# Performance work log

Hardware: AMD Instinct MI355X
Metric: run time of the kernel (lower is better)

## Reference

```python
import jax, jax.numpy as jnp
import numpy as np

N = 50000       # nodes
E = 800000      # edges
F_IN = 128      # num_node_features
H = 128         # hidden_channels
C = 10          # num_classes
G = 512         # graphs in batch


def _glorot(key, shape):
    fan_in, fan_out = shape
    lim = float(np.sqrt(6.0 / (fan_in + fan_out)))
    return jax.random.uniform(key, shape, jnp.float32, -lim, lim)


def setup_inputs() -> dict:
    key = jax.random.key(0)
    ks = jax.random.split(key, 12)
    x = jax.random.normal(ks[0], (N, F_IN), jnp.float32)
    edge_index = jax.random.randint(ks[1], (2, E), 0, N, dtype=jnp.int32).astype(jnp.int64)
    batch = jnp.sort(jax.random.randint(ks[2], (N,), 0, G, dtype=jnp.int32)).astype(jnp.int64)
    return {
        "x": x,
        "edge_index": edge_index,
        "batch": batch,
        "W1": _glorot(ks[3], (F_IN, H)), "b1": jnp.zeros((H,), jnp.float32),
        "W2": _glorot(ks[4], (H, H)),    "b2": jnp.zeros((H,), jnp.float32),
        "W3": _glorot(ks[5], (H, H)),    "b3": jnp.zeros((H,), jnp.float32),
        "W_lin": _glorot(ks[6], (H, C)), "b_lin": jnp.zeros((C,), jnp.float32),
    }


def _gcn_conv(h_in, W, b, src, dst, dis):
    # GCNConv: D^{-1/2} (A + I) D^{-1/2} (X W) + b  (symmetric norm, self-loops)
    h = h_in @ W                                   # [N, H]
    coef = (dis[src] * dis[dst])[:, None]          # [E, 1]
    msg = h[src] * coef                            # gather + scale
    agg = jax.ops.segment_sum(msg, dst, num_segments=N)  # scatter-add at targets
    agg = agg + h * (dis * dis)[:, None]           # self-loop term
    return agg + b


def reference(x, edge_index, batch, W1, b1, W2, b2, W3, b3, W_lin, b_lin):
    src, dst = edge_index[0], edge_index[1]
    # degree with self-loops (counted at aggregation target, PyG convention)
    deg = jax.ops.segment_sum(jnp.ones((E,), jnp.float32), dst, num_segments=N) + 1.0
    dis = jax.lax.rsqrt(deg)

    h = jax.nn.relu(_gcn_conv(x, W1, b1, src, dst, dis))
    h = jax.nn.relu(_gcn_conv(h, W2, b2, src, dst, dis))
    h = _gcn_conv(h, W3, b3, src, dst, dis)

    # global mean pool over graphs
    counts = jax.ops.segment_sum(jnp.ones((N,), jnp.float32), batch, num_segments=G)
    pooled = jax.ops.segment_sum(h, batch, num_segments=G)
    pooled = pooled / jnp.maximum(counts, 1.0)[:, None]

    # dropout(p=0.5, training=False) -> identity
    return pooled @ W_lin + b_lin
```

## Files before the change

kernel.cpp:

```cpp
#include <hip/hip_runtime.h>

#define NN 50000
#define NE 800000
#define FD 128
#define NG 512
#define NC 10

#define NBUCK 196
#define BSHIFT 8
#define BSTRIDE 5120
#define P1_EPB 4096
#define P1_BLOCKS ((NE + P1_EPB - 1) / P1_EPB)

typedef __attribute__((ext_vector_type(8))) short bf16x8;
typedef __attribute__((ext_vector_type(4))) float f32x4;


__device__ __forceinline__ unsigned short f2bf(float f) {
  unsigned int b = __float_as_uint(f);
  b += 0x7FFF + ((b >> 16) & 1);
  return (unsigned short)(b >> 16);
}
__device__ __forceinline__ float blo(unsigned int u) {
  return __uint_as_float(u << 16);
}
__device__ __forceinline__ float bhi(unsigned int u) {
  return __uint_as_float(u & 0xFFFF0000u);
}


__global__ __launch_bounds__(256) void setup_kernel(const float* __restrict__ W1,
                                                    const float* __restrict__ W2,
                                                    const float* __restrict__ W3,
                                                    unsigned short* __restrict__ wf1,
                                                    unsigned short* __restrict__ wf2,
                                                    unsigned short* __restrict__ wf3,
                                                    int* __restrict__ gcursor) {
  int idx = blockIdx.x * 256 + threadIdx.x;
  if (idx < 3 * 16384) {
    int wi = idx >> 14;
    int i = idx & 16383;
    const float* W = (wi == 0) ? W1 : (wi == 1) ? W2 : W3;
    unsigned short* wf = (wi == 0) ? wf1 : (wi == 1) ? wf2 : wf3;
    int j = i & 7, l = (i >> 3) & 63, ks = (i >> 9) & 3, ct = i >> 11;
    int k = ks * 32 + (l >> 4) * 8 + j;
    int c = ct * 16 + (l & 15);
    float w = W[k * 128 + c];
    unsigned int bb = __float_as_uint(w);
    unsigned int bh = bb & 0xFFFF0000u;
    float r = w - __uint_as_float(bh);
    int base = (((ct * 4 + ks) * 2 + 0) * 64 + l) * 8 + j;
    wf[base] = (unsigned short)(bh >> 16);
    wf[base + 512] = f2bf(r);
  } else {
    int t = idx - 3 * 16384;
    if (t < NBUCK) gcursor[t] = t * BSTRIDE;
  }
}
#define SETUP_BLOCKS ((3 * 16384 + NBUCK + 255) / 256)

__global__ __launch_bounds__(1024) void pass1_kernel(const int* __restrict__ ei,
                                                     int* __restrict__ gcursor,
                                                     unsigned int* __restrict__ bucketBuf) {
  __shared__ int bh[NBUCK];
  __shared__ int gbase[NBUCK];
  __shared__ int bcur[NBUCK];

  int tid = threadIdx.x;
  int e0 = blockIdx.x * P1_EPB;
  int ne = NE - e0; if (ne > P1_EPB) ne = P1_EPB;

  if (tid < NBUCK) bh[tid] = 0;
  __syncthreads();

  for (int i = tid; i < ne; i += 1024) {
    int d = ei[NE + e0 + i];
    atomicAdd(&bh[d >> BSHIFT], 1);
  }
  __syncthreads();

  if (tid < NBUCK) {
    bcur[tid] = 0;
    gbase[tid] = (bh[tid] > 0) ? atomicAdd(&gcursor[tid], bh[tid]) : 0;
  }
  __syncthreads();

  for (int i = tid; i < ne; i += 1024) {
    int s = ei[e0 + i];
    int d = ei[NE + e0 + i];
    int b = d >> BSHIFT;
    int p = atomicAdd(&bcur[b], 1);
    bucketBuf[gbase[b] + p] = (unsigned int)s | ((unsigned int)d << 16);
  }
}

__global__ __launch_bounds__(1024) void pass2_kernel(const unsigned int* __restrict__ bucketBuf,
                                                     const int* __restrict__ gcur,
                                                     int* __restrict__ offs,
                                                     float* __restrict__ dis,
                                                     unsigned short* __restrict__ csr) {
  __shared__ unsigned int raw[BSTRIDE];
  __shared__ unsigned short sorted[BSTRIDE];
  __shared__ int h[256], pos[256], cur[256];
  __shared__ int sarr[256];

  int b = blockIdx.x;
  int tid = threadIdx.x;
  int nStart = b << BSHIFT;

  if (tid < 256) sarr[tid] = (tid < NBUCK) ? (gcur[tid] - tid * BSTRIDE) : 0;
  __syncthreads();
  #pragma unroll
  for (int off = 1; off < 256; off <<= 1) {
    int v = 0;
    if (tid < 256 && tid >= off) v = sarr[tid - off];
    __syncthreads();
    if (tid < 256) sarr[tid] += v;
    __syncthreads();
  }
  int cntb = gcur[b] - b * BSTRIDE;
  int cnt = (cntb > BSTRIDE) ? BSTRIDE : cntb;
  int eStart = sarr[b] - cntb;
  if (b == NBUCK - 1 && tid == 0) offs[NN] = sarr[NBUCK - 1];

  for (int i = tid; i < cnt; i += 1024) raw[i] = bucketBuf[(size_t)b * BSTRIDE + i];
  if (tid < 256) h[tid] = 0;
  __syncthreads();

  for (int i = tid; i < cnt; i += 1024) atomicAdd(&h[(raw[i] >> 16) - nStart], 1);
  __syncthreads();

  if (tid < 256) pos[tid] = h[tid];
  __syncthreads();
  #pragma unroll
  for (int off = 1; off < 256; off <<= 1) {
    int v = 0;
    if (tid < 256 && tid >= off) v = pos[tid - off];
    __syncthreads();
    if (tid < 256) pos[tid] += v;
    __syncthreads();
  }
  if (tid < 256) {
    int ex = pos[tid] - h[tid];
    cur[tid] = ex;
    int n = nStart + tid;
    if (n < NN) {
      offs[n] = eStart + ex;
      dis[n] = rsqrtf((float)h[tid] + 1.0f);
    }
  }
  __syncthreads();

  for (int i = tid; i < cnt; i += 1024) {
    unsigned int r = raw[i];
    int d = (int)(r >> 16) - nStart;
    int p = atomicAdd(&cur[d], 1);
    sorted[p] = (unsigned short)(r & 0xFFFFu);
  }
  __syncthreads();

  for (int i = tid; i < cnt; i += 1024) csr[eStart + i] = sorted[i];
}


__global__ __launch_bounds__(256) void gemm_f32_kernel(const float* __restrict__ A,
                                                       const unsigned short* __restrict__ wf,
                                                       const float* __restrict__ dis,
                                                       unsigned short* __restrict__ Hs) {
  __shared__ unsigned short ldsW[32768];
  int tid = threadIdx.x;
  {
    const uint4* src = reinterpret_cast<const uint4*>(wf);
    uint4* dst = reinterpret_cast<uint4*>(ldsW);
    #pragma unroll
    for (int i = 0; i < 16; ++i) dst[tid + i * 256] = src[tid + i * 256];
  }
  __syncthreads();

  int w = tid >> 6, lane = tid & 63;
  int rowbase = blockIdx.x * 128 + w * 32;
  int kgrp = lane >> 4;
  int r0 = rowbase + (lane & 15);
  int r1 = r0 + 16;
  int a0 = (r0 < NN) ? r0 : 0;
  int a1 = (r1 < NN) ? r1 : 0;

  f32x4 acc0[8], acc1[8];
  #pragma unroll
  for (int ct = 0; ct < 8; ++ct) {
    f32x4 z = {0.f, 0.f, 0.f, 0.f};
    acc0[ct] = z; acc1[ct] = z;
  }

  #pragma unroll
  for (int ks = 0; ks < 4; ++ks) {
    bf16x8 ahi0, alo0, ahi1, alo1;
    {
      const float* ap = A + (size_t)a0 * FD + ks * 32 + kgrp * 8;
      float4 v0 = *reinterpret_cast<const float4*>(ap);
      float4 v1 = *reinterpret_cast<const float4*>(ap + 4);
      float a[8] = {v0.x, v0.y, v0.z, v0.w, v1.x, v1.y, v1.z, v1.w};
      #pragma unroll
      for (int j = 0; j < 8; ++j) {
        unsigned int bb = __float_as_uint(a[j]);
        unsigned int bh = bb & 0xFFFF0000u;
        float r = a[j] - __uint_as_float(bh);
        ahi0[j] = (short)(bh >> 16);
        alo0[j] = (short)f2bf(r);
      }
    }
    {
      const float* ap = A + (size_t)a1 * FD + ks * 32 + kgrp * 8;
      float4 v0 = *reinterpret_cast<const float4*>(ap);
      float4 v1 = *reinterpret_cast<const float4*>(ap + 4);
      float a[8] = {v0.x, v0.y, v0.z, v0.w, v1.x, v1.y, v1.z, v1.w};
      #pragma unroll
      for (int j = 0; j < 8; ++j) {
        unsigned int bb = __float_as_uint(a[j]);
        unsigned int bh = bb & 0xFFFF0000u;
        float r = a[j] - __uint_as_float(bh);
        ahi1[j] = (short)(bh >> 16);
        alo1[j] = (short)f2bf(r);
      }
    }
    #pragma unroll
    for (int ct = 0; ct < 8; ++ct) {
      int off = (((ct * 4 + ks) * 2) * 64 + lane) * 8;
      bf16x8 bhiV = *reinterpret_cast<const bf16x8*>(&ldsW[off]);
      bf16x8 bloV = *reinterpret_cast<const bf16x8*>(&ldsW[off + 512]);
      acc0[ct] = __builtin_amdgcn_mfma_f32_16x16x32_bf16(ahi0, bhiV, acc0[ct], 0, 0, 0);
      acc1[ct] = __builtin_amdgcn_mfma_f32_16x16x32_bf16(ahi1, bhiV, acc1[ct], 0, 0, 0);
      acc0[ct] = __builtin_amdgcn_mfma_f32_16x16x32_bf16(alo0, bhiV, acc0[ct], 0, 0, 0);
      acc1[ct] = __builtin_amdgcn_mfma_f32_16x16x32_bf16(alo1, bhiV, acc1[ct], 0, 0, 0);
      acc0[ct] = __builtin_amdgcn_mfma_f32_16x16x32_bf16(ahi0, bloV, acc0[ct], 0, 0, 0);
      acc1[ct] = __builtin_amdgcn_mfma_f32_16x16x32_bf16(ahi1, bloV, acc1[ct], 0, 0, 0);
    }
  }

  int ccol = lane & 15;
  #pragma unroll
  for (int g = 0; g < 2; ++g) {
    int crow0 = rowbase + g * 16 + kgrp * 4;
    #pragma unroll
    for (int i = 0; i < 4; ++i) {
      int r = crow0 + i;
      if (r < NN) {
        float dv = dis[r];
        #pragma unroll
        for (int ct = 0; ct < 8; ++ct) {
          float v = g ? acc1[ct][i] : acc0[ct][i];
          Hs[(size_t)r * FD + ct * 16 + ccol] = f2bf(dv * v);
        }
      }
    }
  }
}


__global__ __launch_bounds__(256) void gemm_bf16_kernel(const unsigned short* __restrict__ Ab,
                                                        const unsigned short* __restrict__ wf,
                                                        const float* __restrict__ dis,
                                                        unsigned short* __restrict__ Hs) {
  __shared__ unsigned short ldsW[32768];
  int tid = threadIdx.x;
  {
    const uint4* src = reinterpret_cast<const uint4*>(wf);
    uint4* dst = reinterpret_cast<uint4*>(ldsW);
    #pragma unroll
    for (int i = 0; i < 16; ++i) dst[tid + i * 256] = src[tid + i * 256];
  }
  __syncthreads();

  int w = tid >> 6, lane = tid & 63;
  int rowbase = blockIdx.x * 128 + w * 32;
  int kgrp = lane >> 4;
  int r0 = rowbase + (lane & 15);
  int r1 = r0 + 16;
  int a0 = (r0 < NN) ? r0 : 0;
  int a1 = (r1 < NN) ? r1 : 0;

  f32x4 acc0[8], acc1[8];
  #pragma unroll
  for (int ct = 0; ct < 8; ++ct) {
    f32x4 z = {0.f, 0.f, 0.f, 0.f};
    acc0[ct] = z; acc1[ct] = z;
  }

  #pragma unroll
  for (int ks = 0; ks < 4; ++ks) {
    bf16x8 av0, av1;
    {
      uint4 u = *reinterpret_cast<const uint4*>(&Ab[(size_t)a0 * FD + ks * 32 + kgrp * 8]);
      unsigned int uu[4] = {u.x, u.y, u.z, u.w};
      #pragma unroll
      for (int p = 0; p < 4; ++p) {
        unsigned short lo16 = (unsigned short)(uu[p] & 0xFFFFu);
        unsigned short hi16 = (unsigned short)(uu[p] >> 16);
        av0[2 * p + 0] = (short)(((short)lo16 < 0) ? 0 : lo16);
        av0[2 * p + 1] = (short)(((short)hi16 < 0) ? 0 : hi16);
      }
    }
    {
      uint4 u = *reinterpret_cast<const uint4*>(&Ab[(size_t)a1 * FD + ks * 32 + kgrp * 8]);
      unsigned int uu[4] = {u.x, u.y, u.z, u.w};
      #pragma unroll
      for (int p = 0; p < 4; ++p) {
        unsigned short lo16 = (unsigned short)(uu[p] & 0xFFFFu);
        unsigned short hi16 = (unsigned short)(uu[p] >> 16);
        av1[2 * p + 0] = (short)(((short)lo16 < 0) ? 0 : lo16);
        av1[2 * p + 1] = (short)(((short)hi16 < 0) ? 0 : hi16);
      }
    }
    #pragma unroll
    for (int ct = 0; ct < 8; ++ct) {
      int off = (((ct * 4 + ks) * 2) * 64 + lane) * 8;
      bf16x8 bhiV = *reinterpret_cast<const bf16x8*>(&ldsW[off]);
      bf16x8 bloV = *reinterpret_cast<const bf16x8*>(&ldsW[off + 512]);
      acc0[ct] = __builtin_amdgcn_mfma_f32_16x16x32_bf16(av0, bhiV, acc0[ct], 0, 0, 0);
      acc1[ct] = __builtin_amdgcn_mfma_f32_16x16x32_bf16(av1, bhiV, acc1[ct], 0, 0, 0);
      acc0[ct] = __builtin_amdgcn_mfma_f32_16x16x32_bf16(av0, bloV, acc0[ct], 0, 0, 0);
      acc1[ct] = __builtin_amdgcn_mfma_f32_16x16x32_bf16(av1, bloV, acc1[ct], 0, 0, 0);
    }
  }

  int ccol = lane & 15;
  #pragma unroll
  for (int g = 0; g < 2; ++g) {
    int crow0 = rowbase + g * 16 + kgrp * 4;
    #pragma unroll
    for (int i = 0; i < 4; ++i) {
      int r = crow0 + i;
      if (r < NN) {
        float dv = dis[r];
        #pragma unroll
        for (int ct = 0; ct < 8; ++ct) {
          float v = g ? acc1[ct][i] : acc0[ct][i];
          Hs[(size_t)r * FD + ct * 16 + ccol] = f2bf(dv * v);
        }
      }
    }
  }
}


#define EDGE8(acc, h)                                        \
  acc[0] += blo(h.x); acc[1] += bhi(h.x);                    \
  acc[2] += blo(h.y); acc[3] += bhi(h.y);                    \
  acc[4] += blo(h.z); acc[5] += bhi(h.z);                    \
  acc[6] += blo(h.w); acc[7] += bhi(h.w);

#define EDGE8M(acc, h, m)                                    \
  acc[0] += m * blo(h.x); acc[1] += m * bhi(h.x);            \
  acc[2] += m * blo(h.y); acc[3] += m * bhi(h.y);            \
  acc[4] += m * blo(h.z); acc[5] += m * bhi(h.z);            \
  acc[6] += m * blo(h.w); acc[7] += m * bhi(h.w);

__global__ __launch_bounds__(256) void agg_edge_kernel(const int* __restrict__ offs,
                                                       const unsigned short* __restrict__ csr,
                                                       const float* __restrict__ dis,
                                                       const unsigned short* __restrict__ Hs,
                                                       const float* __restrict__ bias,
                                                       unsigned short* __restrict__ AGG) {
  int pair = blockIdx.x * 4 + (threadIdx.x >> 6);
  int n0 = pair * 2;
  if (n0 >= NN) return;
  n0 = __builtin_amdgcn_readfirstlane(n0);
  int n1 = n0 + 1;
  int lane = threadIdx.x & 63;
  int q = lane >> 4;
  int ch = (lane & 15) * 8;

  int beg0 = offs[n0], end0 = offs[n0 + 1];
  int beg1 = end0,     end1 = offs[n1 + 1];

  float a0[8], a1[8];
  #pragma unroll
  for (int k = 0; k < 8; ++k) { a0[k] = 0.f; a1[k] = 0.f; }

  if (q == 0) {
    uint4 hn = *reinterpret_cast<const uint4*>(&Hs[(size_t)n0 * FD + ch]);
    EDGE8(a0, hn);
  } else if (q == 1) {
    uint4 hn = *reinterpret_cast<const uint4*>(&Hs[(size_t)n1 * FD + ch]);
    EDGE8(a1, hn);
  }

  int j0 = beg0, j1 = beg1;
  int it = min((end0 - j0) >> 4, (end1 - j1) >> 4);
  for (int t = 0; t < it; ++t) {
    int s00 = csr[j0 + q], s01 = csr[j0 + q + 4], s02 = csr[j0 + q + 8], s03 = csr[j0 + q + 12];
    int s10 = csr[j1 + q], s11 = csr[j1 + q + 4], s12 = csr[j1 + q + 8], s13 = csr[j1 + q + 12];
    uint4 h00 = *reinterpret_cast<const uint4*>(&Hs[(size_t)s00 * FD + ch]);
    uint4 h01 = *reinterpret_cast<const uint4*>(&Hs[(size_t)s01 * FD + ch]);
    uint4 h02 = *reinterpret_cast<const uint4*>(&Hs[(size_t)s02 * FD + ch]);
    uint4 h03 = *reinterpret_cast<const uint4*>(&Hs[(size_t)s03 * FD + ch]);
    uint4 h10 = *reinterpret_cast<const uint4*>(&Hs[(size_t)s10 * FD + ch]);
    uint4 h11 = *reinterpret_cast<const uint4*>(&Hs[(size_t)s11 * FD + ch]);
    uint4 h12 = *reinterpret_cast<const uint4*>(&Hs[(size_t)s12 * FD + ch]);
    uint4 h13 = *reinterpret_cast<const uint4*>(&Hs[(size_t)s13 * FD + ch]);
    EDGE8(a0, h00); EDGE8(a0, h01); EDGE8(a0, h02); EDGE8(a0, h03);
    EDGE8(a1, h10); EDGE8(a1, h11); EDGE8(a1, h12); EDGE8(a1, h13);
    j0 += 16; j1 += 16;
  }
  for (; j0 < end0; j0 += 16) {
    int last = end0 - 1;
    int e0 = j0 + q, e1 = j0 + q + 4, e2 = j0 + q + 8, e3 = j0 + q + 12;
    int i0 = (e0 <= last) ? e0 : 0, i1 = (e1 <= last) ? e1 : 0;
    int i2 = (e2 <= last) ? e2 : 0, i3 = (e3 <= last) ? e3 : 0;
    float m0 = (e0 <= last) ? 1.f : 0.f, m1 = (e1 <= last) ? 1.f : 0.f;
    float m2 = (e2 <= last) ? 1.f : 0.f, m3 = (e3 <= last) ? 1.f : 0.f;
    int s0 = csr[i0], s1 = csr[i1], s2 = csr[i2], s3 = csr[i3];
    uint4 h0 = *reinterpret_cast<const uint4*>(&Hs[(size_t)s0 * FD + ch]);
    uint4 h1 = *reinterpret_cast<const uint4*>(&Hs[(size_t)s1 * FD + ch]);
    uint4 h2 = *reinterpret_cast<const uint4*>(&Hs[(size_t)s2 * FD + ch]);
    uint4 h3 = *reinterpret_cast<const uint4*>(&Hs[(size_t)s3 * FD + ch]);
    EDGE8M(a0, h0, m0); EDGE8M(a0, h1, m1); EDGE8M(a0, h2, m2); EDGE8M(a0, h3, m3);
  }
  for (; j1 < end1; j1 += 16) {
    int last = end1 - 1;
    int e0 = j1 + q, e1 = j1 + q + 4, e2 = j1 + q + 8, e3 = j1 + q + 12;
    int i0 = (e0 <= last) ? e0 : 0, i1 = (e1 <= last) ? e1 : 0;
    int i2 = (e2 <= last) ? e2 : 0, i3 = (e3 <= last) ? e3 : 0;
    float m0 = (e0 <= last) ? 1.f : 0.f, m1 = (e1 <= last) ? 1.f : 0.f;
    float m2 = (e2 <= last) ? 1.f : 0.f, m3 = (e3 <= last) ? 1.f : 0.f;
    int s0 = csr[i0], s1 = csr[i1], s2 = csr[i2], s3 = csr[i3];
    uint4 h0 = *reinterpret_cast<const uint4*>(&Hs[(size_t)s0 * FD + ch]);
    uint4 h1 = *reinterpret_cast<const uint4*>(&Hs[(size_t)s1 * FD + ch]);
    uint4 h2 = *reinterpret_cast<const uint4*>(&Hs[(size_t)s2 * FD + ch]);
    uint4 h3 = *reinterpret_cast<const uint4*>(&Hs[(size_t)s3 * FD + ch]);
    EDGE8M(a1, h0, m0); EDGE8M(a1, h1, m1); EDGE8M(a1, h2, m2); EDGE8M(a1, h3, m3);
  }

  #pragma unroll
  for (int k = 0; k < 8; ++k) {
    float v0 = a0[k];
    v0 += __shfl_xor(v0, 16, 64);
    v0 += __shfl_xor(v0, 32, 64);
    a0[k] = v0;
    float v1 = a1[k];
    v1 += __shfl_xor(v1, 16, 64);
    v1 += __shfl_xor(v1, 32, 64);
    a1[k] = v1;
  }

  if (q < 2) {
    int n = q ? n1 : n0;
    float dn = dis[n];
    const float* acc = q ? a1 : a0;
    float4 b0 = *reinterpret_cast<const float4*>(&bias[ch]);
    float4 b1 = *reinterpret_cast<const float4*>(&bias[ch + 4]);
    float o[8];
    o[0] = b0.x + dn * acc[0]; o[1] = b0.y + dn * acc[1];
    o[2] = b0.z + dn * acc[2]; o[3] = b0.w + dn * acc[3];
    o[4] = b1.x + dn * acc[4]; o[5] = b1.y + dn * acc[5];
    o[6] = b1.z + dn * acc[6]; o[7] = b1.w + dn * acc[7];
    uint4 pk;
    pk.x = (unsigned int)f2bf(o[0]) | ((unsigned int)f2bf(o[1]) << 16);
    pk.y = (unsigned int)f2bf(o[2]) | ((unsigned int)f2bf(o[3]) << 16);
    pk.z = (unsigned int)f2bf(o[4]) | ((unsigned int)f2bf(o[5]) << 16);
    pk.w = (unsigned int)f2bf(o[6]) | ((unsigned int)f2bf(o[7]) << 16);
    *reinterpret_cast<uint4*>(&AGG[(size_t)n * FD + ch]) = pk;
  }
}


__device__ __forceinline__ int lower_bound(const int* __restrict__ b, int n, int key) {
  int lo = 0, hi = n;
  while (lo < hi) {
    int m = (lo + hi) >> 1;
    if (b[m] < key) lo = m + 1; else hi = m;
  }
  return lo;
}

__global__ __launch_bounds__(256) void pool_final_kernel(const unsigned short* __restrict__ AGG,
                                                         const int* __restrict__ batch,
                                                         const float* __restrict__ Wl,
                                                         const float* __restrict__ bl,
                                                         float* __restrict__ out) {
  int g = blockIdx.x;
  int tid = threadIdx.x;
  int lane = tid & 63, w = tid >> 6;
  int start = lower_bound(batch, NN, g);
  int end = lower_bound(batch, NN, g + 1);

  float2 acc = make_float2(0.f, 0.f);
  for (int n = start + w; n < end; n += 4) {
    unsigned int v = *reinterpret_cast<const unsigned int*>(&AGG[(size_t)n * FD + lane * 2]);
    acc.x += blo(v);
    acc.y += bhi(v);
  }
  __shared__ float red[4][FD];
  red[w][lane * 2 + 0] = acc.x;
  red[w][lane * 2 + 1] = acc.y;
  __syncthreads();
  if (w == 0) {
    float px = red[0][lane * 2] + red[1][lane * 2] + red[2][lane * 2] + red[3][lane * 2];
    float py = red[0][lane * 2 + 1] + red[1][lane * 2 + 1] + red[2][lane * 2 + 1] + red[3][lane * 2 + 1];
    float inv = 1.0f / fmaxf((float)(end - start), 1.0f);
    px *= inv; py *= inv;
    float pc[NC];
    #pragma unroll
    for (int c = 0; c < NC; ++c)
      pc[c] = px * Wl[(2 * lane) * NC + c] + py * Wl[(2 * lane + 1) * NC + c];
    #pragma unroll
    for (int off = 32; off > 0; off >>= 1) {
      #pragma unroll
      for (int c = 0; c < NC; ++c) pc[c] += __shfl_down(pc[c], off, 64);
    }
    if (lane == 0) {
      #pragma unroll
      for (int c = 0; c < NC; ++c) out[g * NC + c] = pc[c] + bl[c];
    }
  }
}


extern "C" void kernel_launch(void* const* d_in, const int* in_sizes, int n_in,
                              void* d_out, int out_size, void* d_ws, size_t ws_size,
                              hipStream_t stream) {
  const float* x       = (const float*)d_in[0];
  const int* ei        = (const int*)d_in[1];
  const int* batch     = (const int*)d_in[2];
  const float* W1 = (const float*)d_in[3];
  const float* b1 = (const float*)d_in[4];
  const float* W2 = (const float*)d_in[5];
  const float* b2 = (const float*)d_in[6];
  const float* W3 = (const float*)d_in[7];
  const float* b3 = (const float*)d_in[8];
  const float* Wl = (const float*)d_in[9];
  const float* bl = (const float*)d_in[10];
  float* out = (float*)d_out;

  char* ws = (char*)d_ws;
  size_t o = 0;
  auto alloc = [&](size_t bytes) {
    void* p = ws + o;
    o += bytes;
    o = (o + 255) & ~(size_t)255;
    return p;
  };
  int*   offs   = (int*)  alloc((size_t)(NN + 1) * 4);
  float* dis    = (float*)alloc((size_t)NN * 4);
  int*   gcur   = (int*)  alloc((size_t)NBUCK * 4);
  unsigned int* bucketBuf = (unsigned int*)alloc((size_t)NBUCK * BSTRIDE * 4);
  unsigned short* csr  = (unsigned short*)alloc((size_t)NE * 2 + 64);
  unsigned short* hs   = (unsigned short*)alloc((size_t)NN * FD * 2);
  unsigned short* aggb = (unsigned short*)alloc((size_t)NN * FD * 2);
  unsigned short* wf1 = (unsigned short*)alloc((size_t)2 * FD * FD * 2);
  unsigned short* wf2 = (unsigned short*)alloc((size_t)2 * FD * FD * 2);
  unsigned short* wf3 = (unsigned short*)alloc((size_t)2 * FD * FD * 2);

  setup_kernel<<<SETUP_BLOCKS, 256, 0, stream>>>(W1, W2, W3, wf1, wf2, wf3, gcur);
  pass1_kernel<<<P1_BLOCKS, 1024, 0, stream>>>(ei, gcur, bucketBuf);
  pass2_kernel<<<NBUCK, 1024, 0, stream>>>(bucketBuf, gcur, offs, dis, csr);

  int gemmGrid = (NN + 127) / 128;
  int aggGrid = (NN / 2 + 3) / 4;

  gemm_f32_kernel<<<gemmGrid, 256, 0, stream>>>(x, wf1, dis, hs);
  agg_edge_kernel<<<aggGrid, 256, 0, stream>>>(offs, csr, dis, hs, b1, aggb);
  gemm_bf16_kernel<<<gemmGrid, 256, 0, stream>>>(aggb, wf2, dis, hs);
  agg_edge_kernel<<<aggGrid, 256, 0, stream>>>(offs, csr, dis, hs, b2, aggb);
  gemm_bf16_kernel<<<gemmGrid, 256, 0, stream>>>(aggb, wf3, dis, hs);
  agg_edge_kernel<<<aggGrid, 256, 0, stream>>>(offs, csr, dis, hs, b3, aggb);

  pool_final_kernel<<<NG, 256, 0, stream>>>(aggb, batch, Wl, bl, out);
}
```

Measured before the change: 171.5 us.

## Fuse third-layer edge aggregation into the mean-pool and final linear kernel

The last GCN aggregation is folded into the per-graph pooling kernel. Each block gathers neighbor rows for the nodes of its graph and accumulates them directly into graph sums in fp32, so the bf16 layer-3 output is never written and re-read and one launch disappears. In exchange, the aggregation runs on only 512 blocks with four waves each, so load balance now depends on graph sizes and parallelism drops compared with the node-parallel aggregation kernel.

```diff
diff --git a/kernel.cpp b/kernel.cpp
--- a/kernel.cpp
+++ b/kernel.cpp
@@ -473,36 +473,82 @@
   return lo;
 }
 
-__global__ __launch_bounds__(256) void pool_final_kernel(const unsigned short* __restrict__ AGG,
-                                                         const int* __restrict__ batch,
-                                                         const float* __restrict__ Wl,
-                                                         const float* __restrict__ bl,
-                                                         float* __restrict__ out) {
+__global__ __launch_bounds__(256) void agg_pool_kernel(const int* __restrict__ offs,
+                                                       const unsigned short* __restrict__ csr,
+                                                       const float* __restrict__ dis,
+                                                       const unsigned short* __restrict__ Hs,
+                                                       const float* __restrict__ b3,
+                                                       const int* __restrict__ batch,
+                                                       const float* __restrict__ Wl,
+                                                       const float* __restrict__ bl,
+                                                       float* __restrict__ out) {
   int g = blockIdx.x;
   int tid = threadIdx.x;
-  int lane = tid & 63, w = tid >> 6;
+  int lane = tid & 63;
+  int w = __builtin_amdgcn_readfirstlane(tid >> 6);
+  int q = lane >> 4;
+  int ch = (lane & 15) * 8;
   int start = lower_bound(batch, NN, g);
   int end = lower_bound(batch, NN, g + 1);
 
-  float2 acc = make_float2(0.f, 0.f);
+  float gacc[8];
+  #pragma unroll
+  for (int k = 0; k < 8; ++k) gacc[k] = 0.f;
+
   for (int n = start + w; n < end; n += 4) {
-    unsigned int v = *reinterpret_cast<const unsigned int*>(&AGG[(size_t)n * FD + lane * 2]);
-    acc.x += blo(v);
-    acc.y += bhi(v);
-  }
+    int beg = offs[n], endE = offs[n + 1];
+    float qa[8];
+    #pragma unroll
+    for (int k = 0; k < 8; ++k) qa[k] = 0.f;
+    if (q == 0) {
+      uint4 hn = *reinterpret_cast<const uint4*>(&Hs[(size_t)n * FD + ch]);
+      EDGE8(qa, hn);
+    }
+    int last = endE - 1;
+    for (int j = beg; j < endE; j += 16) {
+      int e0 = j + q, e1 = j + q + 4, e2 = j + q + 8, e3 = j + q + 12;
+      int i0 = (e0 <= last) ? e0 : 0, i1 = (e1 <= last) ? e1 : 0;
+      int i2 = (e2 <= last) ? e2 : 0, i3 = (e3 <= last) ? e3 : 0;
+      float m0 = (e0 <= last) ? 1.f : 0.f, m1 = (e1 <= last) ? 1.f : 0.f;
+      float m2 = (e2 <= last) ? 1.f : 0.f, m3 = (e3 <= last) ? 1.f : 0.f;
+      int s0 = csr[i0], s1 = csr[i1], s2 = csr[i2], s3 = csr[i3];
+      uint4 h0 = *reinterpret_cast<const uint4*>(&Hs[(size_t)s0 * FD + ch]);
+      uint4 h1 = *reinterpret_cast<const uint4*>(&Hs[(size_t)s1 * FD + ch]);
+      uint4 h2 = *reinterpret_cast<const uint4*>(&Hs[(size_t)s2 * FD + ch]);
+      uint4 h3 = *reinterpret_cast<const uint4*>(&Hs[(size_t)s3 * FD + ch]);
+      EDGE8M(qa, h0, m0); EDGE8M(qa, h1, m1); EDGE8M(qa, h2, m2); EDGE8M(qa, h3, m3);
+    }
+    float dn = dis[n];
+    #pragma unroll
+    for (int k = 0; k < 8; ++k) gacc[k] += dn * qa[k];
+  }
+
+  #pragma unroll
+  for (int k = 0; k < 8; ++k) {
+    float v = gacc[k];
+    v += __shfl_xor(v, 16, 64);
+    v += __shfl_xor(v, 32, 64);
+    gacc[k] = v;
+  }
+
   __shared__ float red[4][FD];
-  red[w][lane * 2 + 0] = acc.x;
-  red[w][lane * 2 + 1] = acc.y;
-  __syncthreads();
+  if (q == 0) {
+    #pragma unroll
+    for (int k = 0; k < 8; ++k) red[w][ch + k] = gacc[k];
+  }
+  __syncthreads();
+
   if (w == 0) {
-    float px = red[0][lane * 2] + red[1][lane * 2] + red[2][lane * 2] + red[3][lane * 2];
-    float py = red[0][lane * 2 + 1] + red[1][lane * 2 + 1] + red[2][lane * 2 + 1] + red[3][lane * 2 + 1];
-    float inv = 1.0f / fmaxf((float)(end - start), 1.0f);
-    px *= inv; py *= inv;
+    int cnt = end - start;
+    float inv = (cnt > 0) ? 1.0f / (float)cnt : 0.f;
+    float sel = (cnt > 0) ? 1.f : 0.f;
+    int c0 = lane * 2, c1 = lane * 2 + 1;
+    float px = (red[0][c0] + red[1][c0] + red[2][c0] + red[3][c0]) * inv + sel * b3[c0];
+    float py = (red[0][c1] + red[1][c1] + red[2][c1] + red[3][c1]) * inv + sel * b3[c1];
     float pc[NC];
     #pragma unroll
     for (int c = 0; c < NC; ++c)
-      pc[c] = px * Wl[(2 * lane) * NC + c] + py * Wl[(2 * lane + 1) * NC + c];
+      pc[c] = px * Wl[c0 * NC + c] + py * Wl[c1 * NC + c];
     #pragma unroll
     for (int off = 32; off > 0; off >>= 1) {
       #pragma unroll
@@ -563,7 +609,5 @@
   gemm_bf16_kernel<<<gemmGrid, 256, 0, stream>>>(aggb, wf2, dis, hs);
   agg_edge_kernel<<<aggGrid, 256, 0, stream>>>(offs, csr, dis, hs, b2, aggb);
   gemm_bf16_kernel<<<gemmGrid, 256, 0, stream>>>(aggb, wf3, dis, hs);
-  agg_edge_kernel<<<aggGrid, 256, 0, stream>>>(offs, csr, dis, hs, b3, aggb);
-
-  pool_final_kernel<<<NG, 256, 0, stream>>>(aggb, batch, Wl, bl, out);
-}
+  agg_pool_kernel<<<NG, 256, 0, stream>>>(offs, csr, dis, hs, b3, batch, Wl, bl, out);
+}
```

Result: slower. 187.4 us (+9.3%).
